# Kernel tuning notes

Measured on AMD Instinct MI355X. Metric: run time of the kernel, lower is better.

## Reference

```python
import jax, jax.numpy as jnp
import numpy as np

NUM_CLASSES = 26
PERCENTILE = 95.0
BIG = jnp.float32(1e10)


def _erode(m):
    # scipy-style binary erosion with cross structuring element, border_value=0
    p = jnp.pad(m, 1, constant_values=False)
    return m & p[:-2, 1:-1] & p[2:, 1:-1] & p[1:-1, :-2] & p[1:-1, 2:]


def _boundary(m):
    return m & ~_erode(m)


def _edt(edge):
    # Exact Euclidean distance transform to nearest True pixel of `edge` [H, W].
    # Two-pass separable formulation (rows then columns), fully vectorized.
    H, W = edge.shape
    r = jnp.arange(H)
    rd2 = ((r[:, None] - r[None, :]) ** 2).astype(jnp.float32)  # [H, H']
    # g[i, j] = min over i' with edge[i', j] of (i - i')^2
    g = jnp.min(jnp.where(edge[None, :, :], rd2[:, :, None], BIG), axis=1)  # [H, W]
    c = jnp.arange(W)
    cd2 = ((c[:, None] - c[None, :]) ** 2).astype(jnp.float32)  # [W', W]
    # dt2[i, j] = min over j' of g[i, j'] + (j' - j)^2
    dt2 = jnp.min(g[:, :, None] + cd2[None, :, :], axis=1)  # [H, W]
    return jnp.sqrt(dt2)


def _pct95(dists, mask):
    # np.percentile(dists[mask], 95) with linear interpolation; nan if mask empty
    n = jnp.sum(mask)
    s = jnp.sort(jnp.where(mask, dists, jnp.inf))
    idx = (PERCENTILE / 100.0) * (n.astype(jnp.float32) - 1.0)
    idx = jnp.maximum(idx, 0.0)
    lo = jnp.floor(idx).astype(jnp.int32)
    hi = jnp.ceil(idx).astype(jnp.int32)
    vlo = s[lo]
    vhi = s[hi]
    val = vlo + (vhi - vlo) * (idx - jnp.floor(idx))
    return jnp.where(n > 0, val, jnp.nan)


def _hd_pair(pl, tl, c):
    # 95th-percentile symmetric Hausdorff between pred/target binary masks of class c
    pm = pl == c
    tm = tl == c
    pe = _boundary(pm)
    te = _boundary(tm)
    dt_t = _edt(te)  # distance to target boundary
    dt_p = _edt(pe)  # distance to pred boundary
    d_pt = _pct95(dt_t.ravel(), pe.ravel())  # pred-edge -> target-edge
    d_tp = _pct95(dt_p.ravel(), te.ravel())  # target-edge -> pred-edge
    return jnp.maximum(d_pt, d_tp)


def setup_inputs() -> dict:
    key = jax.random.key(0)
    k1, k2 = jax.random.split(key)
    predicted = jax.random.normal(k1, (2, NUM_CLASSES, 256, 256), dtype=jnp.float32)
    target = jax.random.normal(k2, (2, NUM_CLASSES, 256, 256), dtype=jnp.float32)
    return {"predicted": predicted, "target": target}


def reference(predicted, target):
    probs = jax.nn.softmax(predicted, axis=1)
    pl = jnp.argmax(probs, axis=1)   # [B, H, W]
    tl = jnp.argmax(target, axis=1)  # [B, H, W]

    def per_class(c):
        hd = jax.vmap(lambda p, t: _hd_pair(p, t, c))(pl, tl)  # [B]
        present = jnp.any(tl == c, axis=(1, 2))                # [B]
        return hd, present

    hds, pres = jax.lax.map(per_class, jnp.arange(NUM_CLASSES))  # [C, B]
    presf = pres.astype(jnp.float32)
    num = jnp.sum(jnp.where(pres, hds, 0.0), axis=0)  # [B]
    den = jnp.sum(presf, axis=0)                      # [B]
    batch_means = num / jnp.maximum(den, 1.0)
    valid = den > 0
    total = jnp.sum(jnp.where(valid, batch_means, 0.0)) / jnp.maximum(
        jnp.sum(valid.astype(jnp.float32)), 1.0)
    return jnp.where(jnp.any(valid), total, jnp.inf)
```

## Files before the change

### kernel.cpp

```cpp
#include <hip/hip_runtime.h>
#include <math.h>

#define HW 65536
#define NC 26
#define NB 2

#define PL_OFF    0
#define TL_OFF    131072
#define CNT_OFF   262144
#define RES_OFF   263424
#define BMP_OFF   264192
#define LISTP_OFF 1116160
#define LISTT_OFF 7931904
#define MINP_OFF  14747648
#define MINT_OFF  28379136

__global__ void k_labels(const float4* __restrict__ pred, const float4* __restrict__ targ,
                         uchar4* __restrict__ pl, uchar4* __restrict__ tl,
                         unsigned int* __restrict__ cnt) {
    int tid = threadIdx.x;
    if (blockIdx.x == 0) {
        for (int i = tid; i < 320; i += 128) cnt[i] = 0;
    }
    int idx = blockIdx.x * 128 + tid;
    if (idx >= (NB * HW / 4)) return;
    int b = idx >> 14, q = idx & 16383;
    const float4* p = pred + ((size_t)b * NC << 14) + q;
    const float4* t = targ + ((size_t)b * NC << 14) + q;
    float4 bp = p[0]; uchar4 ap = {0, 0, 0, 0};
    float4 bt = t[0]; uchar4 at = {0, 0, 0, 0};
#pragma unroll
    for (int c = 1; c < NC; ++c) {
        float4 vp = p[(size_t)c << 14];
        if (vp.x > bp.x) { bp.x = vp.x; ap.x = (unsigned char)c; }
        if (vp.y > bp.y) { bp.y = vp.y; ap.y = (unsigned char)c; }
        if (vp.z > bp.z) { bp.z = vp.z; ap.z = (unsigned char)c; }
        if (vp.w > bp.w) { bp.w = vp.w; ap.w = (unsigned char)c; }
        float4 vt = t[(size_t)c << 14];
        if (vt.x > bt.x) { bt.x = vt.x; at.x = (unsigned char)c; }
        if (vt.y > bt.y) { bt.y = vt.y; at.y = (unsigned char)c; }
        if (vt.z > bt.z) { bt.z = vt.z; at.z = (unsigned char)c; }
        if (vt.w > bt.w) { bt.w = vt.w; at.w = (unsigned char)c; }
    }
    pl[idx] = ap;
    tl[idx] = at;
}

__device__ __forceinline__ bool is_boundary(const unsigned char* __restrict__ L, int hw, int c) {
    int y = hw >> 8, x = hw & 255;
    if (y == 0 || y == 255 || x == 0 || x == 255) return true;
    return (int)L[hw - 256] != c || (int)L[hw + 256] != c ||
           (int)L[hw - 1]   != c || (int)L[hw + 1]   != c;
}

__global__ void k_rowbm(const unsigned char* __restrict__ pl,
                        const unsigned char* __restrict__ tl,
                        unsigned int* __restrict__ bmp,
                        unsigned int* __restrict__ cnt,
                        unsigned short* __restrict__ listP,
                        unsigned short* __restrict__ listT) {
    __shared__ unsigned bm[52][8];
    __shared__ unsigned lh[52];
    __shared__ unsigned lb[52];
    int tid = threadIdx.x;
    int b = blockIdx.x >> 8, y = blockIdx.x & 255;
    for (int i = tid; i < 416; i += 256) ((unsigned*)bm)[i] = 0;
    if (tid < 52) lh[tid] = 0;
    __syncthreads();
    const unsigned char* Lp = pl + (b << 16);
    const unsigned char* Lt = tl + (b << 16);
    int hw = (y << 8) | tid;
    int cp = Lp[hw];
    int ct = Lt[hw];
    bool bnp = is_boundary(Lp, hw, cp);
    bool bnt = is_boundary(Lt, hw, ct);
    unsigned rp = 0, rt = 0;
    if (bnp) {
        atomicOr(&bm[cp][tid >> 5], 1u << (tid & 31));
        rp = atomicAdd(&lh[cp], 1u);
    }
    if (bnt) {
        atomicOr(&bm[26 + ct][tid >> 5], 1u << (tid & 31));
        rt = atomicAdd(&lh[26 + ct], 1u);
    }
    __syncthreads();
    for (int i = tid; i < 416; i += 256) {
        int idx = i >> 3, w = i & 7;
        int m = idx < 26 ? 0 : 1;
        int c = idx < 26 ? idx : idx - 26;
        bmp[(((m * 52 + b * 26 + c) << 8) | y) * 8 + w] = bm[idx][w];
    }
    if (tid < 26)
        lb[tid] = lh[tid] ? atomicAdd(&cnt[208 + b * 26 + tid], lh[tid]) : 0u;
    else if (tid < 52)
        lb[tid] = lh[tid] ? atomicAdd(&cnt[260 + b * 26 + (tid - 26)], lh[tid]) : 0u;
    __syncthreads();
    if (bnp) listP[((unsigned)(b * 26 + cp) << 16) + lb[cp] + rp] = (unsigned short)hw;
    if (bnt) listT[((unsigned)(b * 26 + ct) << 16) + lb[26 + ct] + rt] = (unsigned short)hw;
}

__device__ __forceinline__ int row_dx(const unsigned* sb, int r, int xw, int xb) {
    const unsigned* row = sb + r * 9;
    unsigned RM = row[8];
    if (!RM) return 999;
    int dxmin = 999;
    unsigned m = row[xw];
    unsigned le = 0xFFFFFFFFu >> (31 - xb);
    unsigned lm = m & le;
    if (lm) dxmin = xb - 31 + __clz(lm);
    unsigned rmm = m & ~le;
    if (rmm) dxmin = min(dxmin, (__ffs(rmm) - 1) - xb);
    unsigned Lm = RM & ((1u << xw) - 1u);
    if (Lm) {
        int w1 = 31 - __clz(Lm);
        unsigned m1 = row[w1];
        dxmin = min(dxmin, xb + ((xw - w1) << 5) - (31 - __clz(m1)));
    }
    unsigned Rm = RM >> (xw + 1);
    if (Rm) {
        int w2 = xw + __ffs(Rm);
        unsigned m2 = row[w2];
        dxmin = min(dxmin, ((w2 - xw) << 5) + (__ffs(m2) - 1) - xb);
    }
    return dxmin;
}

__global__ __launch_bounds__(512) void k_ring(
        const unsigned int* __restrict__ cnt,
        const unsigned int* __restrict__ bmp,
        const unsigned short* __restrict__ listP,
        const unsigned short* __restrict__ listT,
        float* __restrict__ minP, float* __restrict__ minT) {
    int pair = blockIdx.y;
    int dir = blockIdx.z;
    unsigned ns = cnt[(dir ? 260 : 208) + pair];
    unsigned i0 = blockIdx.x * 512u;
    if (i0 >= ns) return;
    unsigned nt = cnt[(dir ? 208 : 260) + pair];
    if (nt == 0) return;
    const unsigned short* src = (dir ? listT : listP) + ((unsigned)pair << 16);
    float* outv = (dir ? minT : minP) + ((unsigned)pair << 16);

    __shared__ unsigned sb[256 * 9];
    int tid = threadIdx.x;
    {
        const uint4* g4 = (const uint4*)(bmp + ((unsigned)((dir ? 0 : 52) + pair) << 11));
        uint4 v = g4[tid];
        unsigned* row = sb + (tid >> 1) * 9 + ((tid & 1) << 2);
        row[0] = v.x; row[1] = v.y; row[2] = v.z; row[3] = v.w;
    }
    __syncthreads();
    if (tid < 256) {
        const unsigned* row = sb + tid * 9;
        unsigned rm = 0;
#pragma unroll
        for (int w = 0; w < 8; ++w) rm |= (row[w] ? 1u : 0u) << w;
        sb[tid * 9 + 8] = rm;
    }
    __syncthreads();

    unsigned stride = gridDim.x * 512u;
    for (unsigned ib = i0; ib < ns; ib += stride) {
        unsigned i = ib + tid;
        if (i >= ns) continue;
        unsigned h = src[i];
        int x = (int)(h & 255u);
        int sy = (int)(h >> 8);
        int xw = x >> 5, xb = x & 31;
        int best = 0x40000000;
        for (int k = 0; k < 256; ++k) {
            int k2 = k * k;
            if (k2 >= best) break;
            int ra = sy - k, rb = sy + k;
            if (ra < 0 && rb > 255) break;
            if (ra >= 0) {
                int dx = row_dx(sb, ra, xw, xb);
                if (dx < 999) best = min(best, k2 + dx * dx);
            }
            if (k && rb < 256) {
                int dx = row_dx(sb, rb, xw, xb);
                if (dx < 999) best = min(best, k2 + dx * dx);
            }
        }
        outv[i] = (float)best;
    }
}

__global__ void k_select(const unsigned int* __restrict__ cnt,
                         const float* __restrict__ minP, const float* __restrict__ minT,
                         float* __restrict__ res) {
    int pair = blockIdx.x;
    int dir = blockIdx.y;
    unsigned ns = cnt[(dir ? 260 : 208) + pair];
    unsigned nt = cnt[(dir ? 208 : 260) + pair];
    const float* vals = (dir ? minT : minP) + ((unsigned)pair << 16);
    int tid = threadIdx.x;

    if (ns == 0) { if (tid == 0) res[pair * 2 + dir] = nanf(""); return; }
    if (nt == 0) { if (tid == 0) res[pair * 2 + dir] = sqrtf(1e10f); return; }

    __shared__ unsigned hist[1024];
    __shared__ unsigned f1[128], f2[128];
    __shared__ int s_binlo, s_binhi, s_below_lo, s_below_hi;

    for (int i = tid; i < 1024; i += 256) hist[i] = 0;
    __syncthreads();
    for (unsigned i = tid; i < ns; i += 256) {
        int v = (int)vals[i];
        atomicAdd(&hist[v >> 7], 1u);
    }
    __syncthreads();

    float idxf = 0.95f * ((float)ns - 1.0f);
    if (idxf < 0.f) idxf = 0.f;
    int klo = (int)floorf(idxf);
    int khi = (int)ceilf(idxf);

    if (tid == 0) {
        unsigned cum = 0;
        int binlo = -1, binhi = -1, below_lo = 0, below_hi = 0;
        for (int bkt = 0; bkt < 1024; ++bkt) {
            unsigned h = hist[bkt];
            if (binlo < 0 && cum + h > (unsigned)klo) { binlo = bkt; below_lo = (int)cum; }
            if (binhi < 0 && cum + h > (unsigned)khi) { binhi = bkt; below_hi = (int)cum; }
            cum += h;
            if (binhi >= 0) break;
        }
        s_binlo = binlo; s_binhi = binhi; s_below_lo = below_lo; s_below_hi = below_hi;
    }
    __syncthreads();
    if (tid < 128) { f1[tid] = 0; f2[tid] = 0; }
    __syncthreads();
    int binlo = s_binlo, binhi = s_binhi;
    for (unsigned i = tid; i < ns; i += 256) {
        int v = (int)vals[i];
        int bkt = v >> 7;
        if (bkt == binlo) atomicAdd(&f1[v & 127], 1u);
        if (bkt == binhi && binhi != binlo) atomicAdd(&f2[v & 127], 1u);
    }
    __syncthreads();
    if (tid == 0) {
        int rlo = klo - s_below_lo;
        unsigned cum = 0; int d2lo = binlo << 7, d2hi = binhi << 7;
        for (int j = 0; j < 128; ++j) {
            cum += f1[j];
            if ((int)cum > rlo) { d2lo = (binlo << 7) + j; break; }
        }
        if (binhi == binlo) {
            int rhi = khi - s_below_lo;
            cum = 0;
            for (int j = 0; j < 128; ++j) {
                cum += f1[j];
                if ((int)cum > rhi) { d2hi = (binlo << 7) + j; break; }
            }
        } else {
            int rhi = khi - s_below_hi;
            cum = 0;
            for (int j = 0; j < 128; ++j) {
                cum += f2[j];
                if ((int)cum > rhi) { d2hi = (binhi << 7) + j; break; }
            }
        }
        float vlo = sqrtf((float)d2lo);
        float vhi = sqrtf((float)d2hi);
        float frac = idxf - floorf(idxf);
        res[pair * 2 + dir] = vlo + (vhi - vlo) * frac;
    }
}

__global__ void k_final(const unsigned int* __restrict__ cnt, const float* __restrict__ res,
                        float* __restrict__ out) {
    __shared__ float s_res[104];
    __shared__ unsigned s_pres[52];
    int tid = threadIdx.x;
    if (tid < 104) s_res[tid] = res[tid];
    if (tid < 52) s_pres[tid] = cnt[260 + tid];
    __syncthreads();
    if (tid != 0) return;
    float total = 0.f, nvalid = 0.f;
    bool anyv = false;
    for (int b = 0; b < NB; ++b) {
        float num = 0.f, den = 0.f;
        for (int c = 0; c < NC; ++c) {
            int pair = b * NC + c;
            bool present = s_pres[pair] > 0;
            float dpt = s_res[pair * 2];
            float dtp = s_res[pair * 2 + 1];
            float hd;
            if (isnan(dpt) || isnan(dtp)) hd = nanf("");
            else hd = fmaxf(dpt, dtp);
            if (present) { num += hd; den += 1.f; }
        }
        float bm = num / fmaxf(den, 1.f);
        if (den > 0.f) { total += bm; nvalid += 1.f; anyv = true; }
    }
    out[0] = anyv ? (total / fmaxf(nvalid, 1.f)) : INFINITY;
}

extern "C" void kernel_launch(void* const* d_in, const int* in_sizes, int n_in,
                              void* d_out, int out_size, void* d_ws, size_t ws_size,
                              hipStream_t stream) {
    const float* pred = (const float*)d_in[0];
    const float* targ = (const float*)d_in[1];
    float* out = (float*)d_out;
    char* ws = (char*)d_ws;

    unsigned char* pl = (unsigned char*)(ws + PL_OFF);
    unsigned char* tl = (unsigned char*)(ws + TL_OFF);
    unsigned int* cnt = (unsigned int*)(ws + CNT_OFF);
    float* res = (float*)(ws + RES_OFF);
    unsigned int* bmp = (unsigned int*)(ws + BMP_OFF);
    unsigned short* listP = (unsigned short*)(ws + LISTP_OFF);
    unsigned short* listT = (unsigned short*)(ws + LISTT_OFF);
    float* minP = (float*)(ws + MINP_OFF);
    float* minT = (float*)(ws + MINT_OFF);

    k_labels<<<256, 128, 0, stream>>>((const float4*)pred, (const float4*)targ,
                                      (uchar4*)pl, (uchar4*)tl, cnt);
    k_rowbm<<<512, 256, 0, stream>>>(pl, tl, bmp, cnt, listP, listT);
    k_ring<<<dim3(2, 52, 2), 512, 0, stream>>>(cnt, bmp, listP, listT, minP, minT);
    k_select<<<dim3(52, 2), 256, 0, stream>>>(cnt, minP, minT, res);
    k_final<<<1, 128, 0, stream>>>(cnt, res, out);
}
```

Before: 51.07 us.

## Shrink ring-search blocks, widen grid, and unroll row scan by two

The ring-search kernel now runs 256-thread blocks, launches six times as many blocks per pair/direction, and loads the shared bitmap in two passes per thread. The inner nearest-row scan handles two ring distances per iteration and combines four candidate rows before updating the running minimum. The aim is more parallel blocks across CUs and more independent work per iteration for latency hiding. The cost is up to one extra row probe past the early-exit point, and each extra block reloads the bitmap into shared memory.

```diff
diff --git a/kernel.cpp b/kernel.cpp
--- a/kernel.cpp
+++ b/kernel.cpp
@@ -125,7 +125,7 @@
     return dxmin;
 }
 
-__global__ __launch_bounds__(512) void k_ring(
+__global__ __launch_bounds__(256) void k_ring(
         const unsigned int* __restrict__ cnt,
         const unsigned int* __restrict__ bmp,
         const unsigned short* __restrict__ listP,
@@ -134,7 +134,7 @@
     int pair = blockIdx.y;
     int dir = blockIdx.z;
     unsigned ns = cnt[(dir ? 260 : 208) + pair];
-    unsigned i0 = blockIdx.x * 512u;
+    unsigned i0 = blockIdx.x * 256u;
     if (i0 >= ns) return;
     unsigned nt = cnt[(dir ? 208 : 260) + pair];
     if (nt == 0) return;
@@ -145,12 +145,16 @@
     int tid = threadIdx.x;
     {
         const uint4* g4 = (const uint4*)(bmp + ((unsigned)((dir ? 0 : 52) + pair) << 11));
-        uint4 v = g4[tid];
-        unsigned* row = sb + (tid >> 1) * 9 + ((tid & 1) << 2);
-        row[0] = v.x; row[1] = v.y; row[2] = v.z; row[3] = v.w;
-    }
-    __syncthreads();
-    if (tid < 256) {
+#pragma unroll
+        for (int t = 0; t < 2; ++t) {
+            int idx = tid + t * 256;
+            uint4 v = g4[idx];
+            unsigned* row = sb + (idx >> 1) * 9 + ((idx & 1) << 2);
+            row[0] = v.x; row[1] = v.y; row[2] = v.z; row[3] = v.w;
+        }
+    }
+    __syncthreads();
+    {
         const unsigned* row = sb + tid * 9;
         unsigned rm = 0;
 #pragma unroll
@@ -159,7 +163,7 @@
     }
     __syncthreads();
 
-    unsigned stride = gridDim.x * 512u;
+    unsigned stride = gridDim.x * 256u;
     for (unsigned ib = i0; ib < ns; ib += stride) {
         unsigned i = ib + tid;
         if (i >= ns) continue;
@@ -168,19 +172,31 @@
         int sy = (int)(h >> 8);
         int xw = x >> 5, xb = x & 31;
         int best = 0x40000000;
-        for (int k = 0; k < 256; ++k) {
-            int k2 = k * k;
-            if (k2 >= best) break;
-            int ra = sy - k, rb = sy + k;
-            if (ra < 0 && rb > 255) break;
-            if (ra >= 0) {
-                int dx = row_dx(sb, ra, xw, xb);
-                if (dx < 999) best = min(best, k2 + dx * dx);
-            }
-            if (k && rb < 256) {
-                int dx = row_dx(sb, rb, xw, xb);
-                if (dx < 999) best = min(best, k2 + dx * dx);
-            }
+        for (int k = 0; k < 256; k += 2) {
+            int k2a = k * k;
+            if (k2a >= best) break;
+            int raA = sy - k, rbA = sy + k;
+            if (raA < 0 && rbA > 255) break;
+            int k2b = (k + 1) * (k + 1);
+            int raB = raA - 1, rbB = rbA + 1;
+            int c0 = 0x40000000, c1 = 0x40000000, c2 = 0x40000000, c3 = 0x40000000;
+            if (raA >= 0) {
+                int dx = row_dx(sb, raA, xw, xb);
+                if (dx < 999) c0 = k2a + dx * dx;
+            }
+            if (k && rbA < 256) {
+                int dx = row_dx(sb, rbA, xw, xb);
+                if (dx < 999) c1 = k2a + dx * dx;
+            }
+            if (raB >= 0) {
+                int dx = row_dx(sb, raB, xw, xb);
+                if (dx < 999) c2 = k2b + dx * dx;
+            }
+            if (rbB < 256) {
+                int dx = row_dx(sb, rbB, xw, xb);
+                if (dx < 999) c3 = k2b + dx * dx;
+            }
+            best = min(best, min(min(c0, c1), min(c2, c3)));
         }
         outv[i] = (float)best;
     }
@@ -318,7 +334,7 @@
     k_labels<<<256, 128, 0, stream>>>((const float4*)pred, (const float4*)targ,
                                       (uchar4*)pl, (uchar4*)tl, cnt);
     k_rowbm<<<512, 256, 0, stream>>>(pl, tl, bmp, cnt, listP, listT);
-    k_ring<<<dim3(2, 52, 2), 512, 0, stream>>>(cnt, bmp, listP, listT, minP, minT);
+    k_ring<<<dim3(12, 52, 2), 256, 0, stream>>>(cnt, bmp, listP, listT, minP, minT);
     k_select<<<dim3(52, 2), 256, 0, stream>>>(cnt, minP, minT, res);
     k_final<<<1, 128, 0, stream>>>(cnt, res, out);
 }
```

Result: faster. 45.36 us (median of 2 runs) (-11.2%).
